# Optimization experiments

Hardware: AMD Instinct MI355X
Metric: run time of the kernel (lower is better)

Reference implementation:

```python
import jax, jax.numpy as jnp
import numpy as np

N_USERS = 50000
N_ITEMS = 50000
N_ENTITIES = 100000
N_REL = 32
E = 2000000
NI = 1000000
D = 64


def _scatter_mean(src, index, size):
    # scatter_mean: segment sum divided by per-segment count (clamped to 1)
    s = jax.ops.segment_sum(src, index, num_segments=size)
    cnt = jax.ops.segment_sum(jnp.ones((src.shape[0],), src.dtype), index, num_segments=size)
    return s / jnp.maximum(cnt, 1.0)[:, None]


def setup_inputs() -> dict:
    key = jax.random.key(0)
    ks = jax.random.split(key, 8)
    entity_emb = jax.random.normal(ks[0], (N_ENTITIES, D), jnp.float32)
    user_emb = jax.random.normal(ks[1], (N_USERS, D), jnp.float32)
    edge_index = jax.random.randint(ks[2], (2, E), 0, N_ENTITIES)
    edge_type = jax.random.randint(ks[3], (E,), 0, N_REL)
    mat_row = jax.random.randint(ks[4], (NI,), 0, N_USERS)
    mat_col = jax.random.randint(ks[5], (NI,), 0, N_ITEMS)
    mat_val = jnp.ones((NI,), jnp.float32)
    weight = jax.random.normal(ks[6], (N_REL, D), jnp.float32) * 0.1
    k7, k8 = jax.random.split(ks[7])
    gate1_w = jax.random.normal(k7, (D, D), jnp.float32) * 0.125
    gate2_w = jax.random.normal(k8, (D, D), jnp.float32) * 0.125
    return {"entity_emb": entity_emb, "user_emb": user_emb, "edge_index": edge_index,
            "edge_type": edge_type, "mat_row": mat_row, "mat_col": mat_col,
            "mat_val": mat_val, "weight": weight, "gate1_w": gate1_w, "gate2_w": gate2_w}


def reference(entity_emb, user_emb, edge_index, edge_type, mat_row, mat_col, mat_val, weight, gate1_w, gate2_w):
    head, tail = edge_index[0], edge_index[1]
    # KG aggregation: gather tail entity emb, modulate by relation emb, scatter-mean into head
    neigh_relation_emb = entity_emb[tail] * weight[edge_type]          # [E, D]
    entity_agg = _scatter_mean(neigh_relation_emb, head, N_ENTITIES)   # [n_entities, D]

    item_kg_agg = entity_agg[:N_ITEMS]                                 # [n_items, D]
    att_kg_agg = entity_agg[N_ITEMS:]

    # user->item aggregation: gather user emb, modulate by relation 0, scatter-mean into items
    item_neigh_emb = user_emb[mat_row] * weight[0]                     # [NI, D]
    i_u_agg = _scatter_mean(item_neigh_emb, mat_col, N_ITEMS)          # [n_items, D]

    # gated fusion (nn.Linear with no bias: x @ W.T)
    gi = jax.nn.sigmoid(item_kg_agg @ gate1_w.T + i_u_agg @ gate2_w.T)
    item_emb_fusion = gi * item_kg_agg + (1.0 - gi) * i_u_agg          # [n_items, D]

    # user_agg = binary user-item sparse matrix @ item_emb_fusion (values are ones)
    user_agg = jax.ops.segment_sum(item_emb_fusion[mat_col], mat_row, num_segments=N_USERS)

    entity_agg_out = jnp.concatenate([item_emb_fusion, att_kg_agg], axis=0)
    return (entity_agg_out, user_agg)
```

## Files before the change

### kernel.cpp

```cpp
#include <hip/hip_runtime.h>
#include <hip/hip_bf16.h>

#define N_USERS   50000
#define N_ITEMS   50000
#define N_ENT     100000
#define NE        2000000
#define NNI       1000000
#define DD        64

#define PART_E    12500
#define PART_I    6250
#define GROUP     125
#define NG_E      100
#define NG_M      50

#define ECAP_E    262144
#define ECAP_M    131072
#define ST2CAP    2880
#define CHUNK     4096
#define CAPB      640
#define GCAP      96

__global__ __launch_bounds__(256) void bucket_edge_L1(
        const int* __restrict__ head, const int* __restrict__ tail,
        const int* __restrict__ etype,
        int* __restrict__ stK, int* __restrict__ stV, int* __restrict__ cur) {
    __shared__ int bufK[8][CAPB];
    __shared__ int bufV[8][CAPB];
    __shared__ int lcnt[8];
    __shared__ int gbase[8];
    const int tid = threadIdx.x;
    const int lane = tid & 63;
    for (int cs = blockIdx.x * CHUNK; cs < NE; cs += gridDim.x * CHUNK) {
        if (tid < 8) lcnt[tid] = 0;
        __syncthreads();
        const int ce = min(cs + CHUNK, NE);
        for (int i0 = cs; i0 < ce; i0 += 256) {
            const int i = i0 + tid;
            const bool valid = i < ce;
            int h = 0, v = 0, b = 8;
            if (valid) {
                h = __builtin_nontemporal_load(head + i);
                v = __builtin_nontemporal_load(tail + i) |
                    (__builtin_nontemporal_load(etype + i) << 17);
                b = h / PART_E;
            }
            unsigned long long m[8];
            #pragma unroll
            for (int k = 0; k < 8; ++k) m[k] = __ballot(b == k);
            int base8 = 0;
            if (lane < 8) base8 = atomicAdd(&lcnt[lane], (int)__popcll(m[lane]));
            if (valid) {
                const int mybase = __shfl(base8, b);
                const int pos = mybase + (int)__popcll(m[b] & ((1ull << lane) - 1ull));
                if (pos < CAPB) { bufK[b][pos] = h; bufV[b][pos] = v; }
                else {
                    const int gp = atomicAdd(&cur[b], 1);
                    stK[(size_t)b * ECAP_E + gp] = h;
                    stV[(size_t)b * ECAP_E + gp] = v;
                }
            }
        }
        __syncthreads();
        if (tid < 8) gbase[tid] = atomicAdd(&cur[tid], min(lcnt[tid], CAPB));
        __syncthreads();
        for (int b = 0; b < 8; ++b) {
            const int nf = min(lcnt[b], CAPB);
            int* dK = stK + (size_t)b * ECAP_E + gbase[b];
            int* dV = stV + (size_t)b * ECAP_E + gbase[b];
            for (int j = tid; j < nf; j += 256) { dK[j] = bufK[b][j]; dV[j] = bufV[b][j]; }
        }
        __syncthreads();
    }
}

__global__ __launch_bounds__(256) void bucket_mat_L1(
        const int* __restrict__ mrow, const int* __restrict__ mcol,
        int* __restrict__ stC, int* __restrict__ curC,
        int* __restrict__ stR, int* __restrict__ curR) {
    __shared__ int bufc[8][CAPB];
    __shared__ int bufr[8][CAPB];
    __shared__ int lc[8], lr[8], gc[8], gr[8];
    const int tid = threadIdx.x;
    const int lane = tid & 63;
    for (int cs = blockIdx.x * CHUNK; cs < NNI; cs += gridDim.x * CHUNK) {
        if (tid < 8) { lc[tid] = 0; lr[tid] = 0; }
        __syncthreads();
        const int ce = min(cs + CHUNK, NNI);
        for (int i0 = cs; i0 < ce; i0 += 256) {
            const int i = i0 + tid;
            const bool valid = i < ce;
            int r = 0, c = 0, bc = 8, br = 8;
            if (valid) {
                r = __builtin_nontemporal_load(mrow + i);
                c = __builtin_nontemporal_load(mcol + i);
                bc = c / PART_I;
                br = r / PART_I;
            }
            unsigned long long mc[8], mrr[8];
            #pragma unroll
            for (int k = 0; k < 8; ++k) { mc[k] = __ballot(bc == k); mrr[k] = __ballot(br == k); }
            int bc8 = 0, br8 = 0;
            if (lane < 8) {
                bc8 = atomicAdd(&lc[lane], (int)__popcll(mc[lane]));
                br8 = atomicAdd(&lr[lane], (int)__popcll(mrr[lane]));
            }
            if (valid) {
                const unsigned long long lt = (1ull << lane) - 1ull;
                int pos = __shfl(bc8, bc) + (int)__popcll(mc[bc] & lt);
                const int vc = (int)(((unsigned)c << 16) | (unsigned)r);
                if (pos < CAPB) bufc[bc][pos] = vc;
                else stC[(size_t)bc * ECAP_M + atomicAdd(&curC[bc], 1)] = vc;
                pos = __shfl(br8, br) + (int)__popcll(mrr[br] & lt);
                const int vr = (int)(((unsigned)r << 16) | (unsigned)c);
                if (pos < CAPB) bufr[br][pos] = vr;
                else stR[(size_t)br * ECAP_M + atomicAdd(&curR[br], 1)] = vr;
            }
        }
        __syncthreads();
        if (tid < 8)       gc[tid]     = atomicAdd(&curC[tid],     min(lc[tid],     CAPB));
        else if (tid < 16) gr[tid - 8] = atomicAdd(&curR[tid - 8], min(lr[tid - 8], CAPB));
        __syncthreads();
        for (int b = 0; b < 8; ++b) {
            int nf = min(lc[b], CAPB);
            int* d = stC + (size_t)b * ECAP_M + gc[b];
            for (int j = tid; j < nf; j += 256) d[j] = bufc[b][j];
            nf = min(lr[b], CAPB);
            d = stR + (size_t)b * ECAP_M + gr[b];
            for (int j = tid; j < nf; j += 256) d[j] = bufr[b][j];
        }
        __syncthreads();
    }
}

__global__ __launch_bounds__(1024) void bucket_edge_L2(
        const int* __restrict__ stK, const int* __restrict__ stV,
        const int* __restrict__ cur, int* __restrict__ st2,
        int* __restrict__ cur2) {
    __shared__ int buf[NG_E][GCAP];
    __shared__ int lcnt[NG_E];
    const int p = blockIdx.x & 7;
    const int nb = gridDim.x >> 3;
    const int bi = blockIdx.x >> 3;
    const int n = cur[p];
    const int tid = threadIdx.x, w = tid >> 6, lane = tid & 63;
    const int* sK = stK + (size_t)p * ECAP_E;
    const int* sV = stV + (size_t)p * ECAP_E;
    const int pbase = p * PART_E;
    int* cur2p = cur2 + p * NG_E;
    for (int cs = bi * CHUNK; cs < n; cs += nb * CHUNK) {
        for (int t = tid; t < NG_E; t += 1024) lcnt[t] = 0;
        __syncthreads();
        const int ce = min(cs + CHUNK, n);
        for (int i = cs + tid; i < ce; i += 1024) {
            const int local = __builtin_nontemporal_load(sK + i) - pbase;
            const int g = local / GROUP;
            const int rig = local - g * GROUP;
            const int entry = __builtin_nontemporal_load(sV + i) | (rig << 22);
            const int pos = atomicAdd(&lcnt[g], 1);
            if (pos < GCAP) buf[g][pos] = entry;
            else st2[(size_t)(p * NG_E + g) * ST2CAP + atomicAdd(&cur2p[g], 1)] = entry;
        }
        __syncthreads();
        for (int gi = w; gi < NG_E; gi += 16) {
            const int nf = min(lcnt[gi], GCAP);
            int base = 0;
            if (lane == 0 && nf > 0) base = atomicAdd(&cur2p[gi], nf);
            base = __shfl(base, 0);
            int* d = st2 + (size_t)(p * NG_E + gi) * ST2CAP + base;
            for (int j = lane; j < nf; j += 64) d[j] = buf[gi][j];
        }
        __syncthreads();
    }
}

__global__ __launch_bounds__(1024) void bucket_mat_L2(
        const int* __restrict__ st, const int* __restrict__ cur8,
        int* __restrict__ st2, int* __restrict__ cur2) {
    __shared__ int buf[NG_M][GCAP];
    __shared__ int lcnt[NG_M];
    const int p = blockIdx.x & 7;
    const int nb = gridDim.x >> 3;
    const int bi = blockIdx.x >> 3;
    const int n = cur8[p];
    const int tid = threadIdx.x, w = tid >> 6, lane = tid & 63;
    const int* s = st + (size_t)p * ECAP_M;
    const int pbase = p * PART_I;
    int* cur2p = cur2 + p * NG_M;
    for (int cs = bi * CHUNK; cs < n; cs += nb * CHUNK) {
        for (int t = tid; t < NG_M; t += 1024) lcnt[t] = 0;
        __syncthreads();
        const int ce = min(cs + CHUNK, n);
        for (int i = cs + tid; i < ce; i += 1024) {
            const unsigned u = (unsigned)__builtin_nontemporal_load(s + i);
            const int local = (int)(u >> 16) - pbase;
            const int g = local / GROUP;
            const int rig = local - g * GROUP;
            const int entry = (int)(u & 0xFFFFu) | (rig << 16);
            const int pos = atomicAdd(&lcnt[g], 1);
            if (pos < GCAP) buf[g][pos] = entry;
            else st2[(size_t)(p * NG_M + g) * ST2CAP + atomicAdd(&cur2p[g], 1)] = entry;
        }
        __syncthreads();
        for (int gi = w; gi < NG_M; gi += 16) {
            const int nf = min(lcnt[gi], GCAP);
            int base = 0;
            if (lane == 0 && nf > 0) base = atomicAdd(&cur2p[gi], nf);
            base = __shfl(base, 0);
            int* d = st2 + (size_t)(p * NG_M + gi) * ST2CAP + base;
            for (int j = lane; j < nf; j += 64) d[j] = buf[gi][j];
        }
        __syncthreads();
    }
}

template <int SHIFT>
__device__ __forceinline__ void group_sort_body(
        int* __restrict__ st2, const int* __restrict__ cur2, int gg,
        int* __restrict__ row_beg, int* __restrict__ row_cnt) {
    __shared__ int cnt[256];
    __shared__ int loc[GROUP];
    __shared__ int curs[GROUP];
    __shared__ int sorted[ST2CAP];
    const int tid = threadIdx.x;
    const int n = cur2[gg];
    int* s = st2 + (size_t)gg * ST2CAP;
    cnt[tid] = 0;
    __syncthreads();
    for (int i = tid; i < n; i += 256) atomicAdd(&cnt[s[i] >> SHIFT], 1);
    __syncthreads();
    const int x = cnt[tid];
    for (int d = 1; d < 256; d <<= 1) {
        const int v = (tid >= d) ? cnt[tid - d] : 0;
        __syncthreads();
        cnt[tid] += v;
        __syncthreads();
    }
    const int excl = cnt[tid] - x;
    if (tid < GROUP) { loc[tid] = excl; curs[tid] = excl; }
    __syncthreads();
    for (int i = tid; i < n; i += 256) {
        const int e = s[i];
        const int pos = atomicAdd(&curs[e >> SHIFT], 1);
        sorted[pos] = e;
    }
    __syncthreads();
    for (int i = tid; i < n; i += 256) s[i] = sorted[i];
    if (tid < GROUP) {
        row_beg[gg * GROUP + tid] = gg * ST2CAP + loc[tid];
        row_cnt[gg * GROUP + tid] = x;
    }
}

__global__ __launch_bounds__(256) void group_sort_e(
        int* __restrict__ st2, const int* __restrict__ cur2,
        int* __restrict__ row_beg, int* __restrict__ row_cnt) {
    group_sort_body<22>(st2, cur2, blockIdx.x, row_beg, row_cnt);
}

__global__ __launch_bounds__(256) void group_sort_m(
        int* __restrict__ stC2, const int* __restrict__ cur2c,
        int* __restrict__ begc, int* __restrict__ cntc,
        int* __restrict__ stR2, const int* __restrict__ cur2r,
        int* __restrict__ begr, int* __restrict__ cntr) {
    const int b = blockIdx.x;
    if (b < 8 * NG_M) group_sort_body<16>(stC2, cur2c, b, begc, cntc);
    else              group_sort_body<16>(stR2, cur2r, b - 8 * NG_M, begr, cntr);
}

__global__ void pull_entity_kernel(const float* __restrict__ ent,
                                   const float* __restrict__ wgt,
                                   const int* __restrict__ row_beg,
                                   const int* __restrict__ row_cnt,
                                   const int* __restrict__ ids,
                                   float* __restrict__ out) {
    const int lane = threadIdx.x & 63;
    const int wid = (blockIdx.x * blockDim.x + threadIdx.x) >> 6;
    if (wid >= N_ENT) return;
    const int beg = row_beg[wid], nc = row_cnt[wid];
    const int end = beg + nc;
    float acc = 0.f;
    for (int base = beg; base < end; base += 64) {
        const int k = base + lane;
        int v = 0;
        if (k < end) v = ids[k];
        const int nn = min(64, end - base);
        int kk = 0;
        for (; kk + 4 <= nn; kk += 4) {
            const int v0 = __shfl(v, kk),     v1 = __shfl(v, kk + 1);
            const int v2 = __shfl(v, kk + 2), v3 = __shfl(v, kk + 3);
            const float a0 = ent[(size_t)(v0 & 0x1FFFF) * DD + lane] * wgt[((v0 >> 17) & 31) * DD + lane];
            const float a1 = ent[(size_t)(v1 & 0x1FFFF) * DD + lane] * wgt[((v1 >> 17) & 31) * DD + lane];
            const float a2 = ent[(size_t)(v2 & 0x1FFFF) * DD + lane] * wgt[((v2 >> 17) & 31) * DD + lane];
            const float a3 = ent[(size_t)(v3 & 0x1FFFF) * DD + lane] * wgt[((v3 >> 17) & 31) * DD + lane];
            acc += a0 + a1 + a2 + a3;
        }
        for (; kk < nn; ++kk) {
            const int vv = __shfl(v, kk);
            acc += ent[(size_t)(vv & 0x1FFFF) * DD + lane] * wgt[((vv >> 17) & 31) * DD + lane];
        }
    }
    out[(size_t)wid * DD + lane] = acc / fmaxf((float)nc, 1.0f);
}

__global__ void pull_iu_kernel(const float* __restrict__ uemb,
                               const float* __restrict__ wgt,
                               const int* __restrict__ row_beg,
                               const int* __restrict__ row_cnt,
                               const int* __restrict__ ids,
                               float* __restrict__ iu_out) {
    const int lane = threadIdx.x & 63;
    const int wid = (blockIdx.x * blockDim.x + threadIdx.x) >> 6;
    if (wid >= N_ITEMS) return;
    const float w0 = wgt[lane];
    const int beg = row_beg[wid], nc = row_cnt[wid];
    const int end = beg + nc;
    float acc = 0.f;
    for (int base = beg; base < end; base += 64) {
        const int k = base + lane;
        int v = 0;
        if (k < end) v = ids[k];
        const int nn = min(64, end - base);
        int kk = 0;
        for (; kk + 4 <= nn; kk += 4) {
            const int v0 = __shfl(v, kk),     v1 = __shfl(v, kk + 1);
            const int v2 = __shfl(v, kk + 2), v3 = __shfl(v, kk + 3);
            acc += uemb[(size_t)(v0 & 0xFFFF) * DD + lane] + uemb[(size_t)(v1 & 0xFFFF) * DD + lane]
                 + uemb[(size_t)(v2 & 0xFFFF) * DD + lane] + uemb[(size_t)(v3 & 0xFFFF) * DD + lane];
        }
        for (; kk < nn; ++kk) {
            const int vv = __shfl(v, kk);
            acc += uemb[(size_t)(vv & 0xFFFF) * DD + lane];
        }
    }
    iu_out[(size_t)wid * DD + lane] = acc * w0 / fmaxf((float)nc, 1.0f);
}

__global__ void pull_user_kernel(const float* __restrict__ fus,
                                 const int* __restrict__ row_beg,
                                 const int* __restrict__ row_cnt,
                                 const int* __restrict__ ids,
                                 float* __restrict__ uout) {
    const int lane = threadIdx.x & 63;
    const int wid = (blockIdx.x * blockDim.x + threadIdx.x) >> 6;
    if (wid >= N_USERS) return;
    const int beg = row_beg[wid], nc = row_cnt[wid];
    const int end = beg + nc;
    float acc = 0.f;
    for (int base = beg; base < end; base += 64) {
        const int k = base + lane;
        int v = 0;
        if (k < end) v = ids[k];
        const int nn = min(64, end - base);
        int kk = 0;
        for (; kk + 4 <= nn; kk += 4) {
            const int v0 = __shfl(v, kk),     v1 = __shfl(v, kk + 1);
            const int v2 = __shfl(v, kk + 2), v3 = __shfl(v, kk + 3);
            acc += fus[(size_t)(v0 & 0xFFFF) * DD + lane] + fus[(size_t)(v1 & 0xFFFF) * DD + lane]
                 + fus[(size_t)(v2 & 0xFFFF) * DD + lane] + fus[(size_t)(v3 & 0xFFFF) * DD + lane];
        }
        for (; kk < nn; ++kk) {
            const int vv = __shfl(v, kk);
            acc += fus[(size_t)(vv & 0xFFFF) * DD + lane];
        }
    }
    uout[(size_t)wid * DD + lane] = acc;
}

__global__ void gate_fusion_kernel(float* __restrict__ kg_fus,
                                   const float* __restrict__ iu,
                                   const float* __restrict__ g1,
                                   const float* __restrict__ g2) {
    __shared__ float G1[64 * 65];
    __shared__ float G2[64 * 65];
    __shared__ float xs1[4][64];
    __shared__ float xs2[4][64];

    const int tid = threadIdx.x;
    for (int i = tid; i < 64 * 64; i += 256) {
        const int r = i >> 6, c = i & 63;
        G1[r * 65 + c] = g1[i];
        G2[r * 65 + c] = g2[i];
    }

    const int il = tid >> 6;
    const int j = tid & 63;
    const int item = blockIdx.x * 4 + il;

    const float x1 = kg_fus[(size_t)item * DD + j];
    const float x2 = iu[(size_t)item * DD + j];
    xs1[il][j] = x1;
    xs2[il][j] = x2;
    __syncthreads();

    float s = 0.0f;
    #pragma unroll
    for (int k = 0; k < 64; ++k) {
        s += xs1[il][k] * G1[j * 65 + k];
        s += xs2[il][k] * G2[j * 65 + k];
    }
    const float gi = 1.0f / (1.0f + __expf(-s));
    kg_fus[(size_t)item * DD + j] = gi * x1 + (1.0f - gi) * x2;
}

extern "C" void kernel_launch(void* const* d_in, const int* in_sizes, int n_in,
                              void* d_out, int out_size, void* d_ws, size_t ws_size,
                              hipStream_t stream) {
    const float* entity_emb = (const float*)d_in[0];
    const float* user_emb   = (const float*)d_in[1];
    const int*   edge_index = (const int*)d_in[2];
    const int*   edge_type  = (const int*)d_in[3];
    const int*   mat_row    = (const int*)d_in[4];
    const int*   mat_col    = (const int*)d_in[5];
    const float* weight     = (const float*)d_in[7];
    const float* gate1_w    = (const float*)d_in[8];
    const float* gate2_w    = (const float*)d_in[9];

    float* out = (float*)d_out;
    float* out_fusion = out;
    float* out_entity = out;
    float* out_user   = out + (size_t)N_ENT * DD;

    int* W      = (int*)d_ws;
    int* cur_e  = W + 0;
    int* cur_c  = W + 8;
    int* cur_r  = W + 16;
    int* cur2_e = W + 24;
    int* cur2_c = W + 824;
    int* cur2_r = W + 1224;
    int* st_ek  = W + 2048;
    int* st_ev  = W + 2048 + 2097152;
    int* st2_e  = W + 2048 + 2 * 2097152;
    int* stC    = st_ek;
    int* stR    = st_ek + 1048576;
    int* stC2   = st_ev;
    int* stR2   = st2_e;
    int* tabs   = W + 2048 + 2 * 2097152 + 2304000;
    int* beg_e  = tabs;
    int* cnt_e  = tabs + 100000;
    int* beg_c  = tabs + 200000;
    int* cnt_c  = tabs + 250000;
    int* beg_r  = tabs + 300000;
    int* cnt_r  = tabs + 350000;

    const int* head = edge_index;
    const int* tail = edge_index + NE;

    (void)hipMemsetAsync(W, 0, 2048 * sizeof(int), stream);

    bucket_edge_L1<<<512, 256, 0, stream>>>(head, tail, edge_type, st_ek, st_ev, cur_e);
    bucket_edge_L2<<<256, 1024, 0, stream>>>(st_ek, st_ev, cur_e, st2_e, cur2_e);
    group_sort_e<<<800, 256, 0, stream>>>(st2_e, cur2_e, beg_e, cnt_e);
    pull_entity_kernel<<<N_ENT / 4, 256, 0, stream>>>(entity_emb, weight,
                                                      beg_e, cnt_e, st2_e, out_entity);

    bucket_mat_L1<<<256, 256, 0, stream>>>(mat_row, mat_col, stC, cur_c, stR, cur_r);
    bucket_mat_L2<<<256, 1024, 0, stream>>>(stC, cur_c, stC2, cur2_c);
    bucket_mat_L2<<<256, 1024, 0, stream>>>(stR, cur_r, stR2, cur2_r);
    group_sort_m<<<800, 256, 0, stream>>>(stC2, cur2_c, beg_c, cnt_c,
                                          stR2, cur2_r, beg_r, cnt_r);
    pull_iu_kernel<<<N_ITEMS / 4, 256, 0, stream>>>(user_emb, weight,
                                                    beg_c, cnt_c, stC2, out_user);

    gate_fusion_kernel<<<N_ITEMS / 4, 256, 0, stream>>>(out_fusion, out_user,
                                                        gate1_w, gate2_w);

    pull_user_kernel<<<N_USERS / 4, 256, 0, stream>>>(out_fusion,
                                                      beg_r, cnt_r, stR2, out_user);
}
```

Before: 378.5 us.

## Single-pass mat bucketing, merge sort and pull kernels, batch gate fusion

```diff
diff --git a/kernel.cpp b/kernel.cpp
--- a/kernel.cpp
+++ b/kernel.cpp
@@ -9,17 +9,17 @@
 #define DD        64
 
 #define PART_E    12500
-#define PART_I    6250
 #define GROUP     125
 #define NG_E      100
-#define NG_M      50
+#define NGM_ALL   400
 
 #define ECAP_E    262144
-#define ECAP_M    131072
 #define ST2CAP    2880
 #define CHUNK     4096
+#define MCHUNK    8192
 #define CAPB      640
 #define GCAP      96
+#define MCAP      38
 
 __global__ __launch_bounds__(256) void bucket_edge_L1(
         const int* __restrict__ head, const int* __restrict__ tail,
@@ -74,60 +74,41 @@
     }
 }
 
-__global__ __launch_bounds__(256) void bucket_mat_L1(
+__global__ __launch_bounds__(1024) void bucket_mat_direct(
         const int* __restrict__ mrow, const int* __restrict__ mcol,
-        int* __restrict__ stC, int* __restrict__ curC,
-        int* __restrict__ stR, int* __restrict__ curR) {
-    __shared__ int bufc[8][CAPB];
-    __shared__ int bufr[8][CAPB];
-    __shared__ int lc[8], lr[8], gc[8], gr[8];
-    const int tid = threadIdx.x;
-    const int lane = tid & 63;
-    for (int cs = blockIdx.x * CHUNK; cs < NNI; cs += gridDim.x * CHUNK) {
-        if (tid < 8) { lc[tid] = 0; lr[tid] = 0; }
-        __syncthreads();
-        const int ce = min(cs + CHUNK, NNI);
-        for (int i0 = cs; i0 < ce; i0 += 256) {
-            const int i = i0 + tid;
-            const bool valid = i < ce;
-            int r = 0, c = 0, bc = 8, br = 8;
-            if (valid) {
-                r = __builtin_nontemporal_load(mrow + i);
-                c = __builtin_nontemporal_load(mcol + i);
-                bc = c / PART_I;
-                br = r / PART_I;
-            }
-            unsigned long long mc[8], mrr[8];
-            #pragma unroll
-            for (int k = 0; k < 8; ++k) { mc[k] = __ballot(bc == k); mrr[k] = __ballot(br == k); }
-            int bc8 = 0, br8 = 0;
-            if (lane < 8) {
-                bc8 = atomicAdd(&lc[lane], (int)__popcll(mc[lane]));
-                br8 = atomicAdd(&lr[lane], (int)__popcll(mrr[lane]));
-            }
-            if (valid) {
-                const unsigned long long lt = (1ull << lane) - 1ull;
-                int pos = __shfl(bc8, bc) + (int)__popcll(mc[bc] & lt);
-                const int vc = (int)(((unsigned)c << 16) | (unsigned)r);
-                if (pos < CAPB) bufc[bc][pos] = vc;
-                else stC[(size_t)bc * ECAP_M + atomicAdd(&curC[bc], 1)] = vc;
-                pos = __shfl(br8, br) + (int)__popcll(mrr[br] & lt);
-                const int vr = (int)(((unsigned)r << 16) | (unsigned)c);
-                if (pos < CAPB) bufr[br][pos] = vr;
-                else stR[(size_t)br * ECAP_M + atomicAdd(&curR[br], 1)] = vr;
-            }
-        }
-        __syncthreads();
-        if (tid < 8)       gc[tid]     = atomicAdd(&curC[tid],     min(lc[tid],     CAPB));
-        else if (tid < 16) gr[tid - 8] = atomicAdd(&curR[tid - 8], min(lr[tid - 8], CAPB));
-        __syncthreads();
-        for (int b = 0; b < 8; ++b) {
-            int nf = min(lc[b], CAPB);
-            int* d = stC + (size_t)b * ECAP_M + gc[b];
-            for (int j = tid; j < nf; j += 256) d[j] = bufc[b][j];
-            nf = min(lr[b], CAPB);
-            d = stR + (size_t)b * ECAP_M + gr[b];
-            for (int j = tid; j < nf; j += 256) d[j] = bufr[b][j];
+        int* __restrict__ stC2, int* __restrict__ cur2c,
+        int* __restrict__ stR2, int* __restrict__ cur2r) {
+    __shared__ int buf[NGM_ALL][MCAP];
+    __shared__ int lcnt[NGM_ALL];
+    const int dir = blockIdx.x >> 7;
+    const int bi  = blockIdx.x & 127;
+    const int tid = threadIdx.x, w = tid >> 6, lane = tid & 63;
+    const int* key = dir ? mrow : mcol;
+    const int* pay = dir ? mcol : mrow;
+    int* st2  = dir ? stR2 : stC2;
+    int* cur2 = dir ? cur2r : cur2c;
+    for (int cs = bi * MCHUNK; cs < NNI; cs += 128 * MCHUNK) {
+        for (int t = tid; t < NGM_ALL; t += 1024) lcnt[t] = 0;
+        __syncthreads();
+        const int ce = min(cs + MCHUNK, NNI);
+        for (int i = cs + tid; i < ce; i += 1024) {
+            const int k = __builtin_nontemporal_load(key + i);
+            const int p = __builtin_nontemporal_load(pay + i);
+            const int g = k / GROUP;
+            const int rig = k - g * GROUP;
+            const int entry = p | (rig << 16);
+            const int pos = atomicAdd(&lcnt[g], 1);
+            if (pos < MCAP) buf[g][pos] = entry;
+            else st2[(size_t)g * ST2CAP + atomicAdd(&cur2[g], 1)] = entry;
+        }
+        __syncthreads();
+        for (int gi = w; gi < NGM_ALL; gi += 16) {
+            const int nf = min(lcnt[gi], MCAP);
+            int base = 0;
+            if (lane == 0 && nf > 0) base = atomicAdd(&cur2[gi], nf);
+            base = __shfl(base, 0);
+            int* d = st2 + (size_t)gi * ST2CAP + base;
+            for (int j = lane; j < nf; j += 64) d[j] = buf[gi][j];
         }
         __syncthreads();
     }
@@ -174,46 +155,6 @@
     }
 }
 
-__global__ __launch_bounds__(1024) void bucket_mat_L2(
-        const int* __restrict__ st, const int* __restrict__ cur8,
-        int* __restrict__ st2, int* __restrict__ cur2) {
-    __shared__ int buf[NG_M][GCAP];
-    __shared__ int lcnt[NG_M];
-    const int p = blockIdx.x & 7;
-    const int nb = gridDim.x >> 3;
-    const int bi = blockIdx.x >> 3;
-    const int n = cur8[p];
-    const int tid = threadIdx.x, w = tid >> 6, lane = tid & 63;
-    const int* s = st + (size_t)p * ECAP_M;
-    const int pbase = p * PART_I;
-    int* cur2p = cur2 + p * NG_M;
-    for (int cs = bi * CHUNK; cs < n; cs += nb * CHUNK) {
-        for (int t = tid; t < NG_M; t += 1024) lcnt[t] = 0;
-        __syncthreads();
-        const int ce = min(cs + CHUNK, n);
-        for (int i = cs + tid; i < ce; i += 1024) {
-            const unsigned u = (unsigned)__builtin_nontemporal_load(s + i);
-            const int local = (int)(u >> 16) - pbase;
-            const int g = local / GROUP;
-            const int rig = local - g * GROUP;
-            const int entry = (int)(u & 0xFFFFu) | (rig << 16);
-            const int pos = atomicAdd(&lcnt[g], 1);
-            if (pos < GCAP) buf[g][pos] = entry;
-            else st2[(size_t)(p * NG_M + g) * ST2CAP + atomicAdd(&cur2p[g], 1)] = entry;
-        }
-        __syncthreads();
-        for (int gi = w; gi < NG_M; gi += 16) {
-            const int nf = min(lcnt[gi], GCAP);
-            int base = 0;
-            if (lane == 0 && nf > 0) base = atomicAdd(&cur2p[gi], nf);
-            base = __shfl(base, 0);
-            int* d = st2 + (size_t)(p * NG_M + gi) * ST2CAP + base;
-            for (int j = lane; j < nf; j += 64) d[j] = buf[gi][j];
-        }
-        __syncthreads();
-    }
-}
-
 template <int SHIFT>
 __device__ __forceinline__ void group_sort_body(
         int* __restrict__ st2, const int* __restrict__ cur2, int gg,
@@ -252,88 +193,79 @@
     }
 }
 
-__global__ __launch_bounds__(256) void group_sort_e(
-        int* __restrict__ st2, const int* __restrict__ cur2,
-        int* __restrict__ row_beg, int* __restrict__ row_cnt) {
-    group_sort_body<22>(st2, cur2, blockIdx.x, row_beg, row_cnt);
-}
-
-__global__ __launch_bounds__(256) void group_sort_m(
-        int* __restrict__ stC2, const int* __restrict__ cur2c,
-        int* __restrict__ begc, int* __restrict__ cntc,
-        int* __restrict__ stR2, const int* __restrict__ cur2r,
-        int* __restrict__ begr, int* __restrict__ cntr) {
+__global__ __launch_bounds__(256) void sort_all(
+        int* __restrict__ st2_e, const int* __restrict__ cur2_e,
+        int* __restrict__ beg_e, int* __restrict__ cnt_e,
+        int* __restrict__ stC2, const int* __restrict__ cur2_c,
+        int* __restrict__ beg_c, int* __restrict__ cnt_c,
+        int* __restrict__ stR2, const int* __restrict__ cur2_r,
+        int* __restrict__ beg_r, int* __restrict__ cnt_r) {
     const int b = blockIdx.x;
-    if (b < 8 * NG_M) group_sort_body<16>(stC2, cur2c, b, begc, cntc);
-    else              group_sort_body<16>(stR2, cur2r, b - 8 * NG_M, begr, cntr);
-}
-
-__global__ void pull_entity_kernel(const float* __restrict__ ent,
-                                   const float* __restrict__ wgt,
-                                   const int* __restrict__ row_beg,
-                                   const int* __restrict__ row_cnt,
-                                   const int* __restrict__ ids,
-                                   float* __restrict__ out) {
+    if (b < 800)       group_sort_body<22>(st2_e, cur2_e, b, beg_e, cnt_e);
+    else if (b < 1200) group_sort_body<16>(stC2, cur2_c, b - 800, beg_c, cnt_c);
+    else               group_sort_body<16>(stR2, cur2_r, b - 1200, beg_r, cnt_r);
+}
+
+__global__ void pull_ei_kernel(
+        const float* __restrict__ ent, const float* __restrict__ wgt,
+        const int* __restrict__ beg_e, const int* __restrict__ cnt_e,
+        const int* __restrict__ ids_e, float* __restrict__ out_e,
+        const float* __restrict__ uemb,
+        const int* __restrict__ beg_c, const int* __restrict__ cnt_c,
+        const int* __restrict__ ids_c, float* __restrict__ iu_out) {
     const int lane = threadIdx.x & 63;
-    const int wid = (blockIdx.x * blockDim.x + threadIdx.x) >> 6;
-    if (wid >= N_ENT) return;
-    const int beg = row_beg[wid], nc = row_cnt[wid];
-    const int end = beg + nc;
-    float acc = 0.f;
-    for (int base = beg; base < end; base += 64) {
-        const int k = base + lane;
-        int v = 0;
-        if (k < end) v = ids[k];
-        const int nn = min(64, end - base);
-        int kk = 0;
-        for (; kk + 4 <= nn; kk += 4) {
-            const int v0 = __shfl(v, kk),     v1 = __shfl(v, kk + 1);
-            const int v2 = __shfl(v, kk + 2), v3 = __shfl(v, kk + 3);
-            const float a0 = ent[(size_t)(v0 & 0x1FFFF) * DD + lane] * wgt[((v0 >> 17) & 31) * DD + lane];
-            const float a1 = ent[(size_t)(v1 & 0x1FFFF) * DD + lane] * wgt[((v1 >> 17) & 31) * DD + lane];
-            const float a2 = ent[(size_t)(v2 & 0x1FFFF) * DD + lane] * wgt[((v2 >> 17) & 31) * DD + lane];
-            const float a3 = ent[(size_t)(v3 & 0x1FFFF) * DD + lane] * wgt[((v3 >> 17) & 31) * DD + lane];
-            acc += a0 + a1 + a2 + a3;
-        }
-        for (; kk < nn; ++kk) {
-            const int vv = __shfl(v, kk);
-            acc += ent[(size_t)(vv & 0x1FFFF) * DD + lane] * wgt[((vv >> 17) & 31) * DD + lane];
-        }
-    }
-    out[(size_t)wid * DD + lane] = acc / fmaxf((float)nc, 1.0f);
-}
-
-__global__ void pull_iu_kernel(const float* __restrict__ uemb,
-                               const float* __restrict__ wgt,
-                               const int* __restrict__ row_beg,
-                               const int* __restrict__ row_cnt,
-                               const int* __restrict__ ids,
-                               float* __restrict__ iu_out) {
-    const int lane = threadIdx.x & 63;
-    const int wid = (blockIdx.x * blockDim.x + threadIdx.x) >> 6;
-    if (wid >= N_ITEMS) return;
-    const float w0 = wgt[lane];
-    const int beg = row_beg[wid], nc = row_cnt[wid];
-    const int end = beg + nc;
-    float acc = 0.f;
-    for (int base = beg; base < end; base += 64) {
-        const int k = base + lane;
-        int v = 0;
-        if (k < end) v = ids[k];
-        const int nn = min(64, end - base);
-        int kk = 0;
-        for (; kk + 4 <= nn; kk += 4) {
-            const int v0 = __shfl(v, kk),     v1 = __shfl(v, kk + 1);
-            const int v2 = __shfl(v, kk + 2), v3 = __shfl(v, kk + 3);
-            acc += uemb[(size_t)(v0 & 0xFFFF) * DD + lane] + uemb[(size_t)(v1 & 0xFFFF) * DD + lane]
-                 + uemb[(size_t)(v2 & 0xFFFF) * DD + lane] + uemb[(size_t)(v3 & 0xFFFF) * DD + lane];
-        }
-        for (; kk < nn; ++kk) {
-            const int vv = __shfl(v, kk);
-            acc += uemb[(size_t)(vv & 0xFFFF) * DD + lane];
-        }
-    }
-    iu_out[(size_t)wid * DD + lane] = acc * w0 / fmaxf((float)nc, 1.0f);
+    if (blockIdx.x < 25000) {
+        const int wid = (blockIdx.x * 256 + threadIdx.x) >> 6;
+        const int beg = beg_e[wid], nc = cnt_e[wid];
+        const int end = beg + nc;
+        float acc = 0.f;
+        for (int base = beg; base < end; base += 64) {
+            const int k = base + lane;
+            int v = 0;
+            if (k < end) v = ids_e[k];
+            const int nn = min(64, end - base);
+            int kk = 0;
+            for (; kk + 4 <= nn; kk += 4) {
+                const int v0 = __shfl(v, kk),     v1 = __shfl(v, kk + 1);
+                const int v2 = __shfl(v, kk + 2), v3 = __shfl(v, kk + 3);
+                const float a0 = ent[(size_t)(v0 & 0x1FFFF) * DD + lane] * wgt[((v0 >> 17) & 31) * DD + lane];
+                const float a1 = ent[(size_t)(v1 & 0x1FFFF) * DD + lane] * wgt[((v1 >> 17) & 31) * DD + lane];
+                const float a2 = ent[(size_t)(v2 & 0x1FFFF) * DD + lane] * wgt[((v2 >> 17) & 31) * DD + lane];
+                const float a3 = ent[(size_t)(v3 & 0x1FFFF) * DD + lane] * wgt[((v3 >> 17) & 31) * DD + lane];
+                acc += a0 + a1 + a2 + a3;
+            }
+            for (; kk < nn; ++kk) {
+                const int vv = __shfl(v, kk);
+                acc += ent[(size_t)(vv & 0x1FFFF) * DD + lane] * wgt[((vv >> 17) & 31) * DD + lane];
+            }
+        }
+        out_e[(size_t)wid * DD + lane] = acc / fmaxf((float)nc, 1.0f);
+    } else {
+        const int wid = ((blockIdx.x - 25000) * 256 + threadIdx.x) >> 6;
+        if (wid >= N_ITEMS) return;
+        const float w0 = wgt[lane];
+        const int beg = beg_c[wid], nc = cnt_c[wid];
+        const int end = beg + nc;
+        float acc = 0.f;
+        for (int base = beg; base < end; base += 64) {
+            const int k = base + lane;
+            int v = 0;
+            if (k < end) v = ids_c[k];
+            const int nn = min(64, end - base);
+            int kk = 0;
+            for (; kk + 4 <= nn; kk += 4) {
+                const int v0 = __shfl(v, kk),     v1 = __shfl(v, kk + 1);
+                const int v2 = __shfl(v, kk + 2), v3 = __shfl(v, kk + 3);
+                acc += uemb[(size_t)(v0 & 0xFFFF) * DD + lane] + uemb[(size_t)(v1 & 0xFFFF) * DD + lane]
+                     + uemb[(size_t)(v2 & 0xFFFF) * DD + lane] + uemb[(size_t)(v3 & 0xFFFF) * DD + lane];
+            }
+            for (; kk < nn; ++kk) {
+                const int vv = __shfl(v, kk);
+                acc += uemb[(size_t)(vv & 0xFFFF) * DD + lane];
+            }
+        }
+        iu_out[(size_t)wid * DD + lane] = acc * w0 / fmaxf((float)nc, 1.0f);
+    }
 }
 
 __global__ void pull_user_kernel(const float* __restrict__ fus,
@@ -367,10 +299,9 @@
     uout[(size_t)wid * DD + lane] = acc;
 }
 
-__global__ void gate_fusion_kernel(float* __restrict__ kg_fus,
-                                   const float* __restrict__ iu,
-                                   const float* __restrict__ g1,
-                                   const float* __restrict__ g2) {
+__global__ __launch_bounds__(256) void gate_fusion_kernel(
+        float* __restrict__ kg_fus, const float* __restrict__ iu,
+        const float* __restrict__ g1, const float* __restrict__ g2) {
     __shared__ float G1[64 * 65];
     __shared__ float G2[64 * 65];
     __shared__ float xs1[4][64];
@@ -382,25 +313,32 @@
         G1[r * 65 + c] = g1[i];
         G2[r * 65 + c] = g2[i];
     }
-
     const int il = tid >> 6;
     const int j = tid & 63;
-    const int item = blockIdx.x * 4 + il;
-
-    const float x1 = kg_fus[(size_t)item * DD + j];
-    const float x2 = iu[(size_t)item * DD + j];
-    xs1[il][j] = x1;
-    xs2[il][j] = x2;
-    __syncthreads();
-
-    float s = 0.0f;
-    #pragma unroll
-    for (int k = 0; k < 64; ++k) {
-        s += xs1[il][k] * G1[j * 65 + k];
-        s += xs2[il][k] * G2[j * 65 + k];
-    }
-    const float gi = 1.0f / (1.0f + __expf(-s));
-    kg_fus[(size_t)item * DD + j] = gi * x1 + (1.0f - gi) * x2;
+    const int base = blockIdx.x * 32;
+    __syncthreads();
+
+    for (int it = 0; it < 8; ++it) {
+        const int item = base + it * 4 + il;
+        const bool ok = item < N_ITEMS;
+        float x1 = 0.f, x2 = 0.f;
+        if (ok) {
+            x1 = kg_fus[(size_t)item * DD + j];
+            x2 = iu[(size_t)item * DD + j];
+        }
+        xs1[il][j] = x1;
+        xs2[il][j] = x2;
+        __syncthreads();
+        float s = 0.0f;
+        #pragma unroll
+        for (int k = 0; k < 64; ++k) {
+            s += xs1[il][k] * G1[j * 65 + k];
+            s += xs2[il][k] * G2[j * 65 + k];
+        }
+        const float gi = 1.0f / (1.0f + __expf(-s));
+        if (ok) kg_fus[(size_t)item * DD + j] = gi * x1 + (1.0f - gi) * x2;
+        __syncthreads();
+    }
 }
 
 extern "C" void kernel_launch(void* const* d_in, const int* in_sizes, int n_in,
@@ -423,19 +361,15 @@
 
     int* W      = (int*)d_ws;
     int* cur_e  = W + 0;
-    int* cur_c  = W + 8;
-    int* cur_r  = W + 16;
     int* cur2_e = W + 24;
     int* cur2_c = W + 824;
     int* cur2_r = W + 1224;
     int* st_ek  = W + 2048;
-    int* st_ev  = W + 2048 + 2097152;
-    int* st2_e  = W + 2048 + 2 * 2097152;
-    int* stC    = st_ek;
-    int* stR    = st_ek + 1048576;
-    int* stC2   = st_ev;
-    int* stR2   = st2_e;
-    int* tabs   = W + 2048 + 2 * 2097152 + 2304000;
+    int* st_ev  = st_ek + 2097152;
+    int* st2_e  = st_ev + 2097152;
+    int* stC2   = st2_e + 2304000;
+    int* stR2   = stC2 + 1152000;
+    int* tabs   = stR2 + 1152000;
     int* beg_e  = tabs;
     int* cnt_e  = tabs + 100000;
     int* beg_c  = tabs + 200000;
@@ -449,22 +383,17 @@
     (void)hipMemsetAsync(W, 0, 2048 * sizeof(int), stream);
 
     bucket_edge_L1<<<512, 256, 0, stream>>>(head, tail, edge_type, st_ek, st_ev, cur_e);
+    bucket_mat_direct<<<256, 1024, 0, stream>>>(mat_row, mat_col,
+                                                stC2, cur2_c, stR2, cur2_r);
     bucket_edge_L2<<<256, 1024, 0, stream>>>(st_ek, st_ev, cur_e, st2_e, cur2_e);
-    group_sort_e<<<800, 256, 0, stream>>>(st2_e, cur2_e, beg_e, cnt_e);
-    pull_entity_kernel<<<N_ENT / 4, 256, 0, stream>>>(entity_emb, weight,
-                                                      beg_e, cnt_e, st2_e, out_entity);
-
-    bucket_mat_L1<<<256, 256, 0, stream>>>(mat_row, mat_col, stC, cur_c, stR, cur_r);
-    bucket_mat_L2<<<256, 1024, 0, stream>>>(stC, cur_c, stC2, cur2_c);
-    bucket_mat_L2<<<256, 1024, 0, stream>>>(stR, cur_r, stR2, cur2_r);
-    group_sort_m<<<800, 256, 0, stream>>>(stC2, cur2_c, beg_c, cnt_c,
-                                          stR2, cur2_r, beg_r, cnt_r);
-    pull_iu_kernel<<<N_ITEMS / 4, 256, 0, stream>>>(user_emb, weight,
-                                                    beg_c, cnt_c, stC2, out_user);
-
-    gate_fusion_kernel<<<N_ITEMS / 4, 256, 0, stream>>>(out_fusion, out_user,
-                                                        gate1_w, gate2_w);
-
+    sort_all<<<1600, 256, 0, stream>>>(st2_e, cur2_e, beg_e, cnt_e,
+                                       stC2, cur2_c, beg_c, cnt_c,
+                                       stR2, cur2_r, beg_r, cnt_r);
+    pull_ei_kernel<<<37500, 256, 0, stream>>>(entity_emb, weight,
+                                              beg_e, cnt_e, st2_e, out_entity,
+                                              user_emb, beg_c, cnt_c, stC2, out_user);
+    gate_fusion_kernel<<<(N_ITEMS + 31) / 32, 256, 0, stream>>>(out_fusion, out_user,
+                                                                gate1_w, gate2_w);
     pull_user_kernel<<<N_USERS / 4, 256, 0, stream>>>(out_fusion,
                                                       beg_r, cnt_r, stR2, out_user);
 }
```

After: 413.6 us. 1.09x slower.

## Merge group sorts and pull kernels into combined launches, batch gate fusion

Applied to the files above, without the earlier changes.

```diff
diff --git a/kernel.cpp b/kernel.cpp
--- a/kernel.cpp
+++ b/kernel.cpp
@@ -252,88 +252,79 @@
     }
 }
 
-__global__ __launch_bounds__(256) void group_sort_e(
-        int* __restrict__ st2, const int* __restrict__ cur2,
-        int* __restrict__ row_beg, int* __restrict__ row_cnt) {
-    group_sort_body<22>(st2, cur2, blockIdx.x, row_beg, row_cnt);
-}
-
-__global__ __launch_bounds__(256) void group_sort_m(
-        int* __restrict__ stC2, const int* __restrict__ cur2c,
-        int* __restrict__ begc, int* __restrict__ cntc,
-        int* __restrict__ stR2, const int* __restrict__ cur2r,
-        int* __restrict__ begr, int* __restrict__ cntr) {
+__global__ __launch_bounds__(256) void sort_all(
+        int* __restrict__ st2_e, const int* __restrict__ cur2_e,
+        int* __restrict__ beg_e, int* __restrict__ cnt_e,
+        int* __restrict__ stC2, const int* __restrict__ cur2_c,
+        int* __restrict__ beg_c, int* __restrict__ cnt_c,
+        int* __restrict__ stR2, const int* __restrict__ cur2_r,
+        int* __restrict__ beg_r, int* __restrict__ cnt_r) {
     const int b = blockIdx.x;
-    if (b < 8 * NG_M) group_sort_body<16>(stC2, cur2c, b, begc, cntc);
-    else              group_sort_body<16>(stR2, cur2r, b - 8 * NG_M, begr, cntr);
-}
-
-__global__ void pull_entity_kernel(const float* __restrict__ ent,
-                                   const float* __restrict__ wgt,
-                                   const int* __restrict__ row_beg,
-                                   const int* __restrict__ row_cnt,
-                                   const int* __restrict__ ids,
-                                   float* __restrict__ out) {
+    if (b < 800)       group_sort_body<22>(st2_e, cur2_e, b, beg_e, cnt_e);
+    else if (b < 1200) group_sort_body<16>(stC2, cur2_c, b - 800, beg_c, cnt_c);
+    else               group_sort_body<16>(stR2, cur2_r, b - 1200, beg_r, cnt_r);
+}
+
+__global__ void pull_ei_kernel(
+        const float* __restrict__ ent, const float* __restrict__ wgt,
+        const int* __restrict__ beg_e, const int* __restrict__ cnt_e,
+        const int* __restrict__ ids_e, float* __restrict__ out_e,
+        const float* __restrict__ uemb,
+        const int* __restrict__ beg_c, const int* __restrict__ cnt_c,
+        const int* __restrict__ ids_c, float* __restrict__ iu_out) {
     const int lane = threadIdx.x & 63;
-    const int wid = (blockIdx.x * blockDim.x + threadIdx.x) >> 6;
-    if (wid >= N_ENT) return;
-    const int beg = row_beg[wid], nc = row_cnt[wid];
-    const int end = beg + nc;
-    float acc = 0.f;
-    for (int base = beg; base < end; base += 64) {
-        const int k = base + lane;
-        int v = 0;
-        if (k < end) v = ids[k];
-        const int nn = min(64, end - base);
-        int kk = 0;
-        for (; kk + 4 <= nn; kk += 4) {
-            const int v0 = __shfl(v, kk),     v1 = __shfl(v, kk + 1);
-            const int v2 = __shfl(v, kk + 2), v3 = __shfl(v, kk + 3);
-            const float a0 = ent[(size_t)(v0 & 0x1FFFF) * DD + lane] * wgt[((v0 >> 17) & 31) * DD + lane];
-            const float a1 = ent[(size_t)(v1 & 0x1FFFF) * DD + lane] * wgt[((v1 >> 17) & 31) * DD + lane];
-            const float a2 = ent[(size_t)(v2 & 0x1FFFF) * DD + lane] * wgt[((v2 >> 17) & 31) * DD + lane];
-            const float a3 = ent[(size_t)(v3 & 0x1FFFF) * DD + lane] * wgt[((v3 >> 17) & 31) * DD + lane];
-            acc += a0 + a1 + a2 + a3;
-        }
-        for (; kk < nn; ++kk) {
-            const int vv = __shfl(v, kk);
-            acc += ent[(size_t)(vv & 0x1FFFF) * DD + lane] * wgt[((vv >> 17) & 31) * DD + lane];
-        }
-    }
-    out[(size_t)wid * DD + lane] = acc / fmaxf((float)nc, 1.0f);
-}
-
-__global__ void pull_iu_kernel(const float* __restrict__ uemb,
-                               const float* __restrict__ wgt,
-                               const int* __restrict__ row_beg,
-                               const int* __restrict__ row_cnt,
-                               const int* __restrict__ ids,
-                               float* __restrict__ iu_out) {
-    const int lane = threadIdx.x & 63;
-    const int wid = (blockIdx.x * blockDim.x + threadIdx.x) >> 6;
-    if (wid >= N_ITEMS) return;
-    const float w0 = wgt[lane];
-    const int beg = row_beg[wid], nc = row_cnt[wid];
-    const int end = beg + nc;
-    float acc = 0.f;
-    for (int base = beg; base < end; base += 64) {
-        const int k = base + lane;
-        int v = 0;
-        if (k < end) v = ids[k];
-        const int nn = min(64, end - base);
-        int kk = 0;
-        for (; kk + 4 <= nn; kk += 4) {
-            const int v0 = __shfl(v, kk),     v1 = __shfl(v, kk + 1);
-            const int v2 = __shfl(v, kk + 2), v3 = __shfl(v, kk + 3);
-            acc += uemb[(size_t)(v0 & 0xFFFF) * DD + lane] + uemb[(size_t)(v1 & 0xFFFF) * DD + lane]
-                 + uemb[(size_t)(v2 & 0xFFFF) * DD + lane] + uemb[(size_t)(v3 & 0xFFFF) * DD + lane];
-        }
-        for (; kk < nn; ++kk) {
-            const int vv = __shfl(v, kk);
-            acc += uemb[(size_t)(vv & 0xFFFF) * DD + lane];
-        }
-    }
-    iu_out[(size_t)wid * DD + lane] = acc * w0 / fmaxf((float)nc, 1.0f);
+    if (blockIdx.x < 25000) {
+        const int wid = (blockIdx.x * 256 + threadIdx.x) >> 6;
+        const int beg = beg_e[wid], nc = cnt_e[wid];
+        const int end = beg + nc;
+        float acc = 0.f;
+        for (int base = beg; base < end; base += 64) {
+            const int k = base + lane;
+            int v = 0;
+            if (k < end) v = ids_e[k];
+            const int nn = min(64, end - base);
+            int kk = 0;
+            for (; kk + 4 <= nn; kk += 4) {
+                const int v0 = __shfl(v, kk),     v1 = __shfl(v, kk + 1);
+                const int v2 = __shfl(v, kk + 2), v3 = __shfl(v, kk + 3);
+                const float a0 = ent[(size_t)(v0 & 0x1FFFF) * DD + lane] * wgt[((v0 >> 17) & 31) * DD + lane];
+                const float a1 = ent[(size_t)(v1 & 0x1FFFF) * DD + lane] * wgt[((v1 >> 17) & 31) * DD + lane];
+                const float a2 = ent[(size_t)(v2 & 0x1FFFF) * DD + lane] * wgt[((v2 >> 17) & 31) * DD + lane];
+                const float a3 = ent[(size_t)(v3 & 0x1FFFF) * DD + lane] * wgt[((v3 >> 17) & 31) * DD + lane];
+                acc += a0 + a1 + a2 + a3;
+            }
+            for (; kk < nn; ++kk) {
+                const int vv = __shfl(v, kk);
+                acc += ent[(size_t)(vv & 0x1FFFF) * DD + lane] * wgt[((vv >> 17) & 31) * DD + lane];
+            }
+        }
+        out_e[(size_t)wid * DD + lane] = acc / fmaxf((float)nc, 1.0f);
+    } else {
+        const int wid = ((blockIdx.x - 25000) * 256 + threadIdx.x) >> 6;
+        if (wid >= N_ITEMS) return;
+        const float w0 = wgt[lane];
+        const int beg = beg_c[wid], nc = cnt_c[wid];
+        const int end = beg + nc;
+        float acc = 0.f;
+        for (int base = beg; base < end; base += 64) {
+            const int k = base + lane;
+            int v = 0;
+            if (k < end) v = ids_c[k];
+            const int nn = min(64, end - base);
+            int kk = 0;
+            for (; kk + 4 <= nn; kk += 4) {
+                const int v0 = __shfl(v, kk),     v1 = __shfl(v, kk + 1);
+                const int v2 = __shfl(v, kk + 2), v3 = __shfl(v, kk + 3);
+                acc += uemb[(size_t)(v0 & 0xFFFF) * DD + lane] + uemb[(size_t)(v1 & 0xFFFF) * DD + lane]
+                     + uemb[(size_t)(v2 & 0xFFFF) * DD + lane] + uemb[(size_t)(v3 & 0xFFFF) * DD + lane];
+            }
+            for (; kk < nn; ++kk) {
+                const int vv = __shfl(v, kk);
+                acc += uemb[(size_t)(vv & 0xFFFF) * DD + lane];
+            }
+        }
+        iu_out[(size_t)wid * DD + lane] = acc * w0 / fmaxf((float)nc, 1.0f);
+    }
 }
 
 __global__ void pull_user_kernel(const float* __restrict__ fus,
@@ -367,10 +358,9 @@
     uout[(size_t)wid * DD + lane] = acc;
 }
 
-__global__ void gate_fusion_kernel(float* __restrict__ kg_fus,
-                                   const float* __restrict__ iu,
-                                   const float* __restrict__ g1,
-                                   const float* __restrict__ g2) {
+__global__ __launch_bounds__(256) void gate_fusion_kernel(
+        float* __restrict__ kg_fus, const float* __restrict__ iu,
+        const float* __restrict__ g1, const float* __restrict__ g2) {
     __shared__ float G1[64 * 65];
     __shared__ float G2[64 * 65];
     __shared__ float xs1[4][64];
@@ -382,25 +372,32 @@
         G1[r * 65 + c] = g1[i];
         G2[r * 65 + c] = g2[i];
     }
-
     const int il = tid >> 6;
     const int j = tid & 63;
-    const int item = blockIdx.x * 4 + il;
-
-    const float x1 = kg_fus[(size_t)item * DD + j];
-    const float x2 = iu[(size_t)item * DD + j];
-    xs1[il][j] = x1;
-    xs2[il][j] = x2;
+    const int base = blockIdx.x * 32;
     __syncthreads();
 
-    float s = 0.0f;
-    #pragma unroll
-    for (int k = 0; k < 64; ++k) {
-        s += xs1[il][k] * G1[j * 65 + k];
-        s += xs2[il][k] * G2[j * 65 + k];
-    }
-    const float gi = 1.0f / (1.0f + __expf(-s));
-    kg_fus[(size_t)item * DD + j] = gi * x1 + (1.0f - gi) * x2;
+    for (int it = 0; it < 8; ++it) {
+        const int item = base + it * 4 + il;
+        const bool ok = item < N_ITEMS;
+        float x1 = 0.f, x2 = 0.f;
+        if (ok) {
+            x1 = kg_fus[(size_t)item * DD + j];
+            x2 = iu[(size_t)item * DD + j];
+        }
+        xs1[il][j] = x1;
+        xs2[il][j] = x2;
+        __syncthreads();
+        float s = 0.0f;
+        #pragma unroll
+        for (int k = 0; k < 64; ++k) {
+            s += xs1[il][k] * G1[j * 65 + k];
+            s += xs2[il][k] * G2[j * 65 + k];
+        }
+        const float gi = 1.0f / (1.0f + __expf(-s));
+        if (ok) kg_fus[(size_t)item * DD + j] = gi * x1 + (1.0f - gi) * x2;
+        __syncthreads();
+    }
 }
 
 extern "C" void kernel_launch(void* const* d_in, const int* in_sizes, int n_in,
@@ -429,13 +426,13 @@
     int* cur2_c = W + 824;
     int* cur2_r = W + 1224;
     int* st_ek  = W + 2048;
-    int* st_ev  = W + 2048 + 2097152;
-    int* st2_e  = W + 2048 + 2 * 2097152;
+    int* st_ev  = st_ek + 2097152;
     int* stC    = st_ek;
     int* stR    = st_ek + 1048576;
     int* stC2   = st_ev;
-    int* stR2   = st2_e;
-    int* tabs   = W + 2048 + 2 * 2097152 + 2304000;
+    int* st2_e  = st_ev + 2097152;
+    int* stR2   = st2_e + 2304000;
+    int* tabs   = stR2 + 1152000;
     int* beg_e  = tabs;
     int* cnt_e  = tabs + 100000;
     int* beg_c  = tabs + 200000;
@@ -450,21 +447,19 @@
 
     bucket_edge_L1<<<512, 256, 0, stream>>>(head, tail, edge_type, st_ek, st_ev, cur_e);
     bucket_edge_L2<<<256, 1024, 0, stream>>>(st_ek, st_ev, cur_e, st2_e, cur2_e);
-    group_sort_e<<<800, 256, 0, stream>>>(st2_e, cur2_e, beg_e, cnt_e);
-    pull_entity_kernel<<<N_ENT / 4, 256, 0, stream>>>(entity_emb, weight,
-                                                      beg_e, cnt_e, st2_e, out_entity);
 
     bucket_mat_L1<<<256, 256, 0, stream>>>(mat_row, mat_col, stC, cur_c, stR, cur_r);
     bucket_mat_L2<<<256, 1024, 0, stream>>>(stC, cur_c, stC2, cur2_c);
     bucket_mat_L2<<<256, 1024, 0, stream>>>(stR, cur_r, stR2, cur2_r);
-    group_sort_m<<<800, 256, 0, stream>>>(stC2, cur2_c, beg_c, cnt_c,
-                                          stR2, cur2_r, beg_r, cnt_r);
-    pull_iu_kernel<<<N_ITEMS / 4, 256, 0, stream>>>(user_emb, weight,
-                                                    beg_c, cnt_c, stC2, out_user);
-
-    gate_fusion_kernel<<<N_ITEMS / 4, 256, 0, stream>>>(out_fusion, out_user,
-                                                        gate1_w, gate2_w);
-
+
+    sort_all<<<1600, 256, 0, stream>>>(st2_e, cur2_e, beg_e, cnt_e,
+                                       stC2, cur2_c, beg_c, cnt_c,
+                                       stR2, cur2_r, beg_r, cnt_r);
+    pull_ei_kernel<<<37500, 256, 0, stream>>>(entity_emb, weight,
+                                              beg_e, cnt_e, st2_e, out_entity,
+                                              user_emb, beg_c, cnt_c, stC2, out_user);
+    gate_fusion_kernel<<<(N_ITEMS + 31) / 32, 256, 0, stream>>>(out_fusion, out_user,
+                                                                gate1_w, gate2_w);
     pull_user_kernel<<<N_USERS / 4, 256, 0, stream>>>(out_fusion,
                                                       beg_r, cnt_r, stR2, out_user);
 }
```

After: 360.7 us. -4.7%, faster.
